# Kernel tuning notes

Hardware: AMD Instinct MI355X
Metric: run time of the kernel (lower is better)

## Reference

```python
import jax, jax.numpy as jnp
import numpy as np

KH = KW = 3
PAD = 1


def _conv2d(x, w, b):
    y = jax.lax.conv_general_dilated(
        x, w, window_strides=(1, 1), padding=((PAD, PAD), (PAD, PAD)),
        dimension_numbers=("NCHW", "OIHW", "NCHW"))
    return y + b[None, :, None, None]


def _bilinear_sample_one(img, ys, xs):
    # img: [C,H,W]; ys,xs: [K,h,w] absolute sampling coords; zeros outside.
    C, H, W = img.shape
    flat = img.reshape(C, H * W)
    y0 = jnp.floor(ys)
    x0 = jnp.floor(xs)
    wy = ys - y0
    wx = xs - x0

    def gather(yi, xi):
        valid = (yi >= 0) & (yi <= H - 1) & (xi >= 0) & (xi <= W - 1)
        yc = jnp.clip(yi, 0, H - 1).astype(jnp.int32)
        xc = jnp.clip(xi, 0, W - 1).astype(jnp.int32)
        idx = (yc * W + xc).reshape(-1)
        v = jnp.take(flat, idx, axis=1).reshape((C,) + yi.shape)
        return v * valid.astype(img.dtype)

    v00 = gather(y0, x0)
    v01 = gather(y0, x0 + 1)
    v10 = gather(y0 + 1, x0)
    v11 = gather(y0 + 1, x0 + 1)
    return (v00 * (1 - wy) * (1 - wx) + v01 * (1 - wy) * wx
            + v10 * wy * (1 - wx) + v11 * wy * wx)  # [C,K,h,w]


def deform_conv2d(x, offset, weight, bias):
    # x: [B,C,H,W]; offset: [B,2K,h,w] with (dy,dx) per tap; stride 1, pad 1.
    B, C, H, W = x.shape
    h, w = offset.shape[2], offset.shape[3]
    K = KH * KW
    off = offset.reshape(B, K, 2, h, w)
    ky = (jnp.arange(K) // KW - PAD).astype(x.dtype)  # tap row displacement
    kx = (jnp.arange(K) % KW - PAD).astype(x.dtype)
    ii = jnp.arange(h, dtype=x.dtype)[None, :, None]
    jj = jnp.arange(w, dtype=x.dtype)[None, None, :]
    ys = ii - PAD + ky[:, None, None] + off[:, :, 0]  # [B,K,h,w]
    xs = jj - PAD + kx[:, None, None] + off[:, :, 1]
    sampled = jax.vmap(_bilinear_sample_one)(x, ys, xs)  # [B,C,K,h,w]
    Co = weight.shape[0]
    out = jnp.einsum('ock,bckhw->bohw', weight.reshape(Co, C, K), sampled)
    return out + bias[None, :, None, None]


def setup_inputs() -> dict:
    key = jax.random.key(0)
    ks = jax.random.split(key, 5)
    B, C, H, W = 4, 64, 128, 128
    x = jax.random.normal(ks[0], (B, C, H, W), dtype=jnp.float32)
    w_off = jax.random.normal(ks[1], (4, C, KH, KW), dtype=jnp.float32) * 0.05
    b_off = jnp.zeros((4,), dtype=jnp.float32)
    weight = jax.random.normal(ks[2], (C, C, KH, KW), dtype=jnp.float32) * 0.05
    bias = jnp.zeros((C,), dtype=jnp.float32)
    # base_offset: canonical 3x3 tap displacements, layout (dy,dx) per tap.
    ky = np.repeat(np.arange(KH) - PAD, KW).astype(np.float32)
    kx = np.tile(np.arange(KW) - PAD, KH).astype(np.float32)
    base = np.stack([ky, kx], axis=1).reshape(-1)  # [18]
    base_offset = jnp.asarray(np.broadcast_to(base[None, :, None, None], (1, 18, H, W)).copy())
    idx = np.arange(18)
    mask1 = jnp.asarray(idx % 2 == 0)  # y coords -> scale1
    mask2 = jnp.asarray(idx % 2 == 1)  # x coords -> scale2
    return {"x": x, "w_off": w_off, "b_off": b_off, "weight": weight,
            "bias": bias, "base_offset": base_offset, "mask1": mask1, "mask2": mask2}


def reference(x, w_off, b_off, weight, bias, base_offset, mask1, mask2):
    off = _conv2d(x, w_off, b_off)  # [B,4,h,w]
    scale1 = jax.nn.relu(off[:, 2:3]) + 1.0  # [B,1,h,w]
    scale2 = jax.nn.relu(off[:, 3:4]) + 1.0
    shift = jnp.tile(off[:, :2], (1, KH * KW, 1, 1))  # [B,18,h,w]
    # scaled_offset[:, mask1] = base*scale1 ; scaled_offset[:, mask2] = base*scale2
    scale_full = jnp.where(mask1[None, :, None, None], scale1, scale2)  # [B,18,h,w]
    offset = base_offset * scale_full - base_offset + shift
    return deform_conv2d(x, offset, weight, bias)
```

## Files before the change

kernel.cpp:

```cpp
#include <hip/hip_runtime.h>

#define Hd 128
#define Wd 128
#define Cd 64
#define COd 64
#define Bd 4
#define HWd (Hd*Wd)

typedef __attribute__((ext_vector_type(8))) _Float16 half8;
typedef __attribute__((ext_vector_type(2))) _Float16 h2;
typedef __attribute__((ext_vector_type(4))) float    f32x4;

__device__ __align__(16) _Float16 g_wh[COd*576];
__device__ __align__(16) _Float16 g_woffh[16*576];
__device__ float4 g_offs[Bd*HWd];
__device__ __align__(16) unsigned short g_xt[(size_t)Bd*HWd*Cd];

static __device__ __forceinline__ unsigned cvtpkh(float lo, float hi) {
    unsigned r;
    asm("v_cvt_pkrtz_f16_f32 %0, %1, %2" : "=v"(r) : "v"(lo), "v"(hi));
    return r;
}
static __device__ __forceinline__ h2 ash2(unsigned u) {
    union { unsigned u; h2 h; } x; x.u = u; return x.h;
}
static __device__ __forceinline__ unsigned ash2u(h2 h) {
    union { h2 h; unsigned u; } x; x.h = h; return x.u;
}

__global__ __launch_bounds__(256) void k_prep(const float* __restrict__ x,
                                              const float* __restrict__ weight,
                                              const float* __restrict__ w_off) {
    int bid = blockIdx.x;
    if (bid < 512) {
        int b = bid >> 7, y = bid & 127;
        int px = threadIdx.x & 127;
        int h  = threadIdx.x >> 7;
        const float* xb = x + (size_t)b*Cd*HWd + y*Wd + px;
        unsigned short* ob = g_xt + ((size_t)(b*HWd) + y*Wd + px)*Cd + h*32;
        #pragma unroll
        for (int oct = 0; oct < 4; ++oct) {
            unsigned pk[4];
            #pragma unroll
            for (int e = 0; e < 4; ++e) {
                float v0 = xb[(size_t)(h*32 + oct*8 + 2*e    )*HWd];
                float v1 = xb[(size_t)(h*32 + oct*8 + 2*e + 1)*HWd];
                pk[e] = cvtpkh(v0, v1);
            }
            *(uint4*)(ob + oct*8) = make_uint4(pk[0], pk[1], pk[2], pk[3]);
        }
    } else if (bid < 656) {
        int g = (bid - 512)*256 + threadIdx.x;
        if (g < COd*576) {
            int co = g / 576, k = g % 576;
            int t = k >> 6, c = k & 63;
            g_wh[g] = (_Float16)weight[(co*Cd + c)*9 + t];
        }
    } else {
        int g = (bid - 656)*256 + threadIdx.x;
        if (g < 16*576) {
            int row = g / 576, k = g % 576;
            int t = k >> 6, c = k & 63;
            g_woffh[g] = (row < 4) ? (_Float16)w_off[(row*Cd + c)*9 + t] : (_Float16)0.f;
        }
    }
}

__global__ __launch_bounds__(256) void k_offs(const float* __restrict__ b_off) {
    int orig = blockIdx.x;
    int xcd = orig & 7, slot = orig >> 3;
    int g = xcd*2 + (slot >> 6);
    int s = slot & 63;
    int b  = g >> 2;
    int i  = (g & 3)*32 + (s >> 1);
    int j0 = (s & 1) << 6;

    int w  = threadIdx.x >> 6;
    int l  = threadIdx.x & 63;
    int pc = l & 15, q = l >> 4;
    int j  = j0 + w*16 + pc;

    const unsigned short* xb = g_xt + (size_t)b*HWd*Cd;
    const _Float16* arow = g_woffh + pc*576 + q*8;

    f32x4 acc = {0.f, 0.f, 0.f, 0.f};
    #pragma unroll
    for (int t = 0; t < 9; ++t) {
        int yy = i + t/3 - 1, xx = j + t%3 - 1;
        bool ok = (yy >= 0) & (yy <= 127) & (xx >= 0) & (xx <= 127);
        const unsigned short* p = xb + (size_t)(yy*Wd + xx)*Cd + q*8;
        uint4 u0 = ok ? *(const uint4*)p        : make_uint4(0,0,0,0);
        uint4 u1 = ok ? *(const uint4*)(p + 32) : make_uint4(0,0,0,0);
        half8 b0 = *(half8*)&u0;
        half8 b1 = *(half8*)&u1;
        half8 a0 = *(const half8*)(arow + (2*t    )*32);
        half8 a1 = *(const half8*)(arow + (2*t + 1)*32);
        acc = __builtin_amdgcn_mfma_f32_16x16x32_f16(a0, b0, acc, 0, 0, 0);
        acc = __builtin_amdgcn_mfma_f32_16x16x32_f16(a1, b1, acc, 0, 0, 0);
    }
    if (q == 0) {
        float o0 = acc[0] + b_off[0];
        float o1 = acc[1] + b_off[1];
        float o2 = fmaxf(acc[2] + b_off[2], 0.f) + 1.f;
        float o3 = fmaxf(acc[3] + b_off[3], 0.f) + 1.f;
        g_offs[(b*Hd + i)*Wd + j] = make_float4(o0, o1, o2, o3);
    }
}

#define GATHER(T, U00, U01, U10, U11, H00, H01, H10, H11)                         \
    {                                                                             \
        float ys = (float)(i - 1) + (float)((T)/3 - 1)*s1v + off0;                \
        float xs = (float)(jA - 1) + (float)((T)%3 - 1)*s2v + off1;               \
        float y0f = floorf(ys), x0f = floorf(xs);                                 \
        float wy = ys - y0f, wx = xs - x0f;                                       \
        float vy0 = (y0f >=  0.f && y0f <= 127.f) ? 1.f : 0.f;                    \
        float vy1 = (y0f >= -1.f && y0f <= 126.f) ? 1.f : 0.f;                    \
        float vx0 = (x0f >=  0.f && x0f <= 127.f) ? 1.f : 0.f;                    \
        float vx1 = (x0f >= -1.f && x0f <= 126.f) ? 1.f : 0.f;                    \
        float w00 = (1.f-wy)*(1.f-wx)*vy0*vx0, w01 = (1.f-wy)*wx*vy0*vx1;         \
        float w10 = wy*(1.f-wx)*vy1*vx0,       w11 = wy*wx*vy1*vx1;               \
        H00 = ash2(cvtpkh(w00, w00)); H01 = ash2(cvtpkh(w01, w01));               \
        H10 = ash2(cvtpkh(w10, w10)); H11 = ash2(cvtpkh(w11, w11));               \
        int iy0 = min(max((int)y0f,     0), 127), iy1 = min(max((int)y0f+1,0),127);\
        int ix0 = min(max((int)x0f,     0), 127), ix1 = min(max((int)x0f+1,0),127);\
        U00 = *(const uint4*)(xb + (size_t)(iy0*Wd + ix0)*Cd + oct*8);            \
        U01 = *(const uint4*)(xb + (size_t)(iy0*Wd + ix1)*Cd + oct*8);            \
        U10 = *(const uint4*)(xb + (size_t)(iy1*Wd + ix0)*Cd + oct*8);            \
        U11 = *(const uint4*)(xb + (size_t)(iy1*Wd + ix1)*Cd + oct*8);            \
    }

#define PACK_STORE(BUF, U00, U01, U10, U11, H00, H01, H10, H11)                   \
    {                                                                             \
        unsigned a00[4] = {U00.x,U00.y,U00.z,U00.w};                              \
        unsigned a01[4] = {U01.x,U01.y,U01.z,U01.w};                              \
        unsigned a10[4] = {U10.x,U10.y,U10.z,U10.w};                              \
        unsigned a11[4] = {U11.x,U11.y,U11.z,U11.w};                              \
        unsigned pk[4];                                                           \
        _Pragma("unroll")                                                         \
        for (int e = 0; e < 4; ++e) {                                             \
            h2 r = ash2(a00[e])*H00 + ash2(a01[e])*H01                            \
                 + ash2(a10[e])*H10 + ash2(a11[e])*H11;                           \
            pk[e] = ash2u(r);                                                     \
        }                                                                         \
        lds_b[(((BUF)*2 + par)*2 + nt)*64 + slotA] = make_uint4(pk[0],pk[1],pk[2],pk[3]); \
    }

__global__ __launch_bounds__(256) void k_deform(const float* __restrict__ bias,
                                                float* __restrict__ out) {
    __shared__ uint4 lds_b[2*2*2*64];
    int orig = blockIdx.x;
    int xcd = orig & 7, slotB = orig >> 3;
    int g = xcd*2 + (slotB >> 7);
    int s = slotB & 127;
    int b = g >> 2;
    int i = (g & 3)*32 + (s >> 2);
    int j0 = (s & 3) << 5;

    int w = threadIdx.x >> 6, l = threadIdx.x & 63;
    int oct = l & 7, px8 = l >> 3;
    int pxl = w*8 + px8;
    int jA  = j0 + pxl;
    int nt = pxl >> 4, pcA = pxl & 15, qA = oct & 3, par = oct >> 2;
    int slotA = (pcA ^ (qA << 1)) + (qA << 4);
    int pcB = l & 15, qB = l >> 4;
    int physl = (pcB ^ (qB << 1)) + (qB << 4);
    const _Float16* wrow = g_wh + (size_t)(w*16 + pcB)*576 + qB*8;

    const unsigned short* xb = g_xt + (size_t)b*HWd*Cd;
    float4 o4 = g_offs[(b*Hd + i)*Wd + jA];
    float off0 = o4.x, off1 = o4.y, s1v = o4.z, s2v = o4.w;

    f32x4 acc0 = {0.f,0.f,0.f,0.f};
    f32x4 acc1 = {0.f,0.f,0.f,0.f};

    uint4 gc00, gc01, gc10, gc11, gn00, gn01, gn10, gn11;
    h2 hc00, hc01, hc10, hc11, hn00, hn01, hn10, hn11;
    half8 ac0, ac1, an0, an1;

    GATHER(0, gc00, gc01, gc10, gc11, hc00, hc01, hc10, hc11);
    ac0 = *(const half8*)(wrow + 0*32);
    ac1 = *(const half8*)(wrow + 1*32);

    #pragma unroll
    for (int t = 0; t < 9; ++t) {
        if (t < 8) {
            GATHER(t+1, gn00, gn01, gn10, gn11, hn00, hn01, hn10, hn11);
            an0 = *(const half8*)(wrow + (2*t + 2)*32);
            an1 = *(const half8*)(wrow + (2*t + 3)*32);
        }
        PACK_STORE(t & 1, gc00, gc01, gc10, gc11, hc00, hc01, hc10, hc11);
        __syncthreads();
        {
            half8 b00 = *(const half8*)&lds_b[(((t&1)*2 + 0)*2 + 0)*64 + physl];
            half8 b01 = *(const half8*)&lds_b[(((t&1)*2 + 0)*2 + 1)*64 + physl];
            half8 b10 = *(const half8*)&lds_b[(((t&1)*2 + 1)*2 + 0)*64 + physl];
            half8 b11 = *(const half8*)&lds_b[(((t&1)*2 + 1)*2 + 1)*64 + physl];
            acc0 = __builtin_amdgcn_mfma_f32_16x16x32_f16(ac0, b00, acc0, 0, 0, 0);
            acc1 = __builtin_amdgcn_mfma_f32_16x16x32_f16(ac0, b01, acc1, 0, 0, 0);
            acc0 = __builtin_amdgcn_mfma_f32_16x16x32_f16(ac1, b10, acc0, 0, 0, 0);
            acc1 = __builtin_amdgcn_mfma_f32_16x16x32_f16(ac1, b11, acc1, 0, 0, 0);
        }
        if (t < 8) {
            gc00 = gn00; gc01 = gn01; gc10 = gn10; gc11 = gn11;
            hc00 = hn00; hc01 = hn01; hc10 = hn10; hc11 = hn11;
            ac0 = an0; ac1 = an1;
        }
    }

    #pragma unroll
    for (int rr = 0; rr < 4; ++rr) {
        int co = w*16 + qB*4 + rr;
        float bco = bias[co];
        size_t base = ((size_t)(b*COd + co)*Hd + i)*Wd + j0;
        out[base + pcB]      = acc0[rr] + bco;
        out[base + 16 + pcB] = acc1[rr] + bco;
    }
}

extern "C" void kernel_launch(void* const* d_in, const int* in_sizes, int n_in,
                              void* d_out, int out_size, void* d_ws, size_t ws_size,
                              hipStream_t stream) {
    const float* x      = (const float*)d_in[0];
    const float* w_off  = (const float*)d_in[1];
    const float* b_off  = (const float*)d_in[2];
    const float* weight = (const float*)d_in[3];
    const float* bias   = (const float*)d_in[4];
    float* out = (float*)d_out;

    hipLaunchKernelGGL(k_prep,   dim3(692),  dim3(256), 0, stream, x, weight, w_off);
    hipLaunchKernelGGL(k_offs,   dim3(1024), dim3(256), 0, stream, b_off);
    hipLaunchKernelGGL(k_deform, dim3(2048), dim3(256), 0, stream, bias, out);
}
```

Before: 59.68 us.

## Fuse offset conv into deform kernel with per-wave tiles and no block barrier

Merges the offset-prediction conv and the deformable conv into one kernel. Each wave computes offsets for its own 16 pixels with MFMA and passes them to the sampling lanes by shuffle, so the global offsets buffer and one launch go away. Each wave now owns 16 pixels across all 64 output channels and uses a private swizzled LDS region, which removes the block-wide __syncthreads. In exchange, weight A-fragments are reloaded from global memory for each tap and channel group, and register pressure rises under launch bounds of 4 blocks.

```diff
diff --git a/kernel.cpp b/kernel.cpp
--- a/kernel.cpp
+++ b/kernel.cpp
@@ -13,7 +13,6 @@
 
 __device__ __align__(16) _Float16 g_wh[COd*576];
 __device__ __align__(16) _Float16 g_woffh[16*576];
-__device__ float4 g_offs[Bd*HWd];
 __device__ __align__(16) unsigned short g_xt[(size_t)Bd*HWd*Cd];
 
 static __device__ __forceinline__ unsigned cvtpkh(float lo, float hi) {
@@ -66,7 +65,10 @@
     }
 }
 
-__global__ __launch_bounds__(256) void k_offs(const float* __restrict__ b_off) {
+__global__ __launch_bounds__(256, 4) void k_main(const float* __restrict__ b_off,
+                                                 const float* __restrict__ bias,
+                                                 float* __restrict__ out) {
+    __shared__ uint4 lds[4*2*128];
     int orig = blockIdx.x;
     int xcd = orig & 7, slot = orig >> 3;
     int g = xcd*2 + (slot >> 6);
@@ -75,145 +77,139 @@
     int i  = (g & 3)*32 + (s >> 1);
     int j0 = (s & 1) << 6;
 
-    int w  = threadIdx.x >> 6;
-    int l  = threadIdx.x & 63;
+    int w = threadIdx.x >> 6, l = threadIdx.x & 63;
+    int p0 = j0 + w*16;
+    const unsigned short* xb = g_xt + (size_t)b*HWd*Cd;
+    uint4* lw = lds + w*256;
+
     int pc = l & 15, q = l >> 4;
-    int j  = j0 + w*16 + pc;
-
-    const unsigned short* xb = g_xt + (size_t)b*HWd*Cd;
-    const _Float16* arow = g_woffh + pc*576 + q*8;
-
-    f32x4 acc = {0.f, 0.f, 0.f, 0.f};
+
+    f32x4 oacc = {0.f, 0.f, 0.f, 0.f};
+    {
+        int jh = p0 + pc;
+        const _Float16* arow = g_woffh + pc*576 + q*8;
+        #pragma unroll
+        for (int t = 0; t < 9; ++t) {
+            int yy = i + t/3 - 1, xx = jh + t%3 - 1;
+            bool ok = (yy >= 0) & (yy <= 127) & (xx >= 0) & (xx <= 127);
+            const unsigned short* p = xb + (size_t)(yy*Wd + xx)*Cd + q*8;
+            uint4 u0 = ok ? *(const uint4*)p        : make_uint4(0,0,0,0);
+            uint4 u1 = ok ? *(const uint4*)(p + 32) : make_uint4(0,0,0,0);
+            half8 a0 = *(const half8*)(arow + (2*t    )*32);
+            half8 a1 = *(const half8*)(arow + (2*t + 1)*32);
+            oacc = __builtin_amdgcn_mfma_f32_16x16x32_f16(a0, *(half8*)&u0, oacc, 0, 0, 0);
+            oacc = __builtin_amdgcn_mfma_f32_16x16x32_f16(a1, *(half8*)&u1, oacc, 0, 0, 0);
+        }
+    }
+    int oct = l & 7, px8 = l >> 3;
+    int s0i = px8, s1i = 8 + px8;
+    float off0_0 = __shfl(oacc[0], s0i, 64) + b_off[0];
+    float off1_0 = __shfl(oacc[1], s0i, 64) + b_off[1];
+    float sc1_0  = fmaxf(__shfl(oacc[2], s0i, 64) + b_off[2], 0.f) + 1.f;
+    float sc2_0  = fmaxf(__shfl(oacc[3], s0i, 64) + b_off[3], 0.f) + 1.f;
+    float off0_1 = __shfl(oacc[0], s1i, 64) + b_off[0];
+    float off1_1 = __shfl(oacc[1], s1i, 64) + b_off[1];
+    float sc1_1  = fmaxf(__shfl(oacc[2], s1i, 64) + b_off[2], 0.f) + 1.f;
+    float sc2_1  = fmaxf(__shfl(oacc[3], s1i, 64) + b_off[3], 0.f) + 1.f;
+
+    int jr0 = p0 + px8, jr1 = p0 + 8 + px8;
+    int swz = px8 & 7;
+
+    f32x4 accm[4];
+    #pragma unroll
+    for (int cg = 0; cg < 4; ++cg) accm[cg] = (f32x4){0.f, 0.f, 0.f, 0.f};
+
     #pragma unroll
     for (int t = 0; t < 9; ++t) {
-        int yy = i + t/3 - 1, xx = j + t%3 - 1;
-        bool ok = (yy >= 0) & (yy <= 127) & (xx >= 0) & (xx <= 127);
-        const unsigned short* p = xb + (size_t)(yy*Wd + xx)*Cd + q*8;
-        uint4 u0 = ok ? *(const uint4*)p        : make_uint4(0,0,0,0);
-        uint4 u1 = ok ? *(const uint4*)(p + 32) : make_uint4(0,0,0,0);
-        half8 b0 = *(half8*)&u0;
-        half8 b1 = *(half8*)&u1;
-        half8 a0 = *(const half8*)(arow + (2*t    )*32);
-        half8 a1 = *(const half8*)(arow + (2*t + 1)*32);
-        acc = __builtin_amdgcn_mfma_f32_16x16x32_f16(a0, b0, acc, 0, 0, 0);
-        acc = __builtin_amdgcn_mfma_f32_16x16x32_f16(a1, b1, acc, 0, 0, 0);
-    }
-    if (q == 0) {
-        float o0 = acc[0] + b_off[0];
-        float o1 = acc[1] + b_off[1];
-        float o2 = fmaxf(acc[2] + b_off[2], 0.f) + 1.f;
-        float o3 = fmaxf(acc[3] + b_off[3], 0.f) + 1.f;
-        g_offs[(b*Hd + i)*Wd + j] = make_float4(o0, o1, o2, o3);
-    }
-}
-
-#define GATHER(T, U00, U01, U10, U11, H00, H01, H10, H11)                         \
-    {                                                                             \
-        float ys = (float)(i - 1) + (float)((T)/3 - 1)*s1v + off0;                \
-        float xs = (float)(jA - 1) + (float)((T)%3 - 1)*s2v + off1;               \
-        float y0f = floorf(ys), x0f = floorf(xs);                                 \
-        float wy = ys - y0f, wx = xs - x0f;                                       \
-        float vy0 = (y0f >=  0.f && y0f <= 127.f) ? 1.f : 0.f;                    \
-        float vy1 = (y0f >= -1.f && y0f <= 126.f) ? 1.f : 0.f;                    \
-        float vx0 = (x0f >=  0.f && x0f <= 127.f) ? 1.f : 0.f;                    \
-        float vx1 = (x0f >= -1.f && x0f <= 126.f) ? 1.f : 0.f;                    \
-        float w00 = (1.f-wy)*(1.f-wx)*vy0*vx0, w01 = (1.f-wy)*wx*vy0*vx1;         \
-        float w10 = wy*(1.f-wx)*vy1*vx0,       w11 = wy*wx*vy1*vx1;               \
-        H00 = ash2(cvtpkh(w00, w00)); H01 = ash2(cvtpkh(w01, w01));               \
-        H10 = ash2(cvtpkh(w10, w10)); H11 = ash2(cvtpkh(w11, w11));               \
-        int iy0 = min(max((int)y0f,     0), 127), iy1 = min(max((int)y0f+1,0),127);\
-        int ix0 = min(max((int)x0f,     0), 127), ix1 = min(max((int)x0f+1,0),127);\
-        U00 = *(const uint4*)(xb + (size_t)(iy0*Wd + ix0)*Cd + oct*8);            \
-        U01 = *(const uint4*)(xb + (size_t)(iy0*Wd + ix1)*Cd + oct*8);            \
-        U10 = *(const uint4*)(xb + (size_t)(iy1*Wd + ix0)*Cd + oct*8);            \
-        U11 = *(const uint4*)(xb + (size_t)(iy1*Wd + ix1)*Cd + oct*8);            \
-    }
-
-#define PACK_STORE(BUF, U00, U01, U10, U11, H00, H01, H10, H11)                   \
-    {                                                                             \
-        unsigned a00[4] = {U00.x,U00.y,U00.z,U00.w};                              \
-        unsigned a01[4] = {U01.x,U01.y,U01.z,U01.w};                              \
-        unsigned a10[4] = {U10.x,U10.y,U10.z,U10.w};                              \
-        unsigned a11[4] = {U11.x,U11.y,U11.z,U11.w};                              \
-        unsigned pk[4];                                                           \
-        _Pragma("unroll")                                                         \
-        for (int e = 0; e < 4; ++e) {                                             \
-            h2 r = ash2(a00[e])*H00 + ash2(a01[e])*H01                            \
-                 + ash2(a10[e])*H10 + ash2(a11[e])*H11;                           \
-            pk[e] = ash2u(r);                                                     \
-        }                                                                         \
-        lds_b[(((BUF)*2 + par)*2 + nt)*64 + slotA] = make_uint4(pk[0],pk[1],pk[2],pk[3]); \
-    }
-
-__global__ __launch_bounds__(256) void k_deform(const float* __restrict__ bias,
-                                                float* __restrict__ out) {
-    __shared__ uint4 lds_b[2*2*2*64];
-    int orig = blockIdx.x;
-    int xcd = orig & 7, slotB = orig >> 3;
-    int g = xcd*2 + (slotB >> 7);
-    int s = slotB & 127;
-    int b = g >> 2;
-    int i = (g & 3)*32 + (s >> 2);
-    int j0 = (s & 3) << 5;
-
-    int w = threadIdx.x >> 6, l = threadIdx.x & 63;
-    int oct = l & 7, px8 = l >> 3;
-    int pxl = w*8 + px8;
-    int jA  = j0 + pxl;
-    int nt = pxl >> 4, pcA = pxl & 15, qA = oct & 3, par = oct >> 2;
-    int slotA = (pcA ^ (qA << 1)) + (qA << 4);
-    int pcB = l & 15, qB = l >> 4;
-    int physl = (pcB ^ (qB << 1)) + (qB << 4);
-    const _Float16* wrow = g_wh + (size_t)(w*16 + pcB)*576 + qB*8;
-
-    const unsigned short* xb = g_xt + (size_t)b*HWd*Cd;
-    float4 o4 = g_offs[(b*Hd + i)*Wd + jA];
-    float off0 = o4.x, off1 = o4.y, s1v = o4.z, s2v = o4.w;
-
-    f32x4 acc0 = {0.f,0.f,0.f,0.f};
-    f32x4 acc1 = {0.f,0.f,0.f,0.f};
-
-    uint4 gc00, gc01, gc10, gc11, gn00, gn01, gn10, gn11;
-    h2 hc00, hc01, hc10, hc11, hn00, hn01, hn10, hn11;
-    half8 ac0, ac1, an0, an1;
-
-    GATHER(0, gc00, gc01, gc10, gc11, hc00, hc01, hc10, hc11);
-    ac0 = *(const half8*)(wrow + 0*32);
-    ac1 = *(const half8*)(wrow + 1*32);
+        const float ky = (float)(t/3 - 1), kx = (float)(t%3 - 1);
+        uint4 u00, u01, u10, u11, v00, v01, v10, v11;
+        h2 H00, H01, H10, H11, G00, G01, G10, G11;
+        {
+            float ys = (float)(i - 1) + ky*sc1_0 + off0_0;
+            float xs = (float)(jr0 - 1) + kx*sc2_0 + off1_0;
+            float y0f = floorf(ys), x0f = floorf(xs);
+            float wy = ys - y0f, wx = xs - x0f;
+            float vy0 = (y0f >=  0.f && y0f <= 127.f) ? 1.f : 0.f;
+            float vy1 = (y0f >= -1.f && y0f <= 126.f) ? 1.f : 0.f;
+            float vx0 = (x0f >=  0.f && x0f <= 127.f) ? 1.f : 0.f;
+            float vx1 = (x0f >= -1.f && x0f <= 126.f) ? 1.f : 0.f;
+            float w00 = (1.f-wy)*(1.f-wx)*vy0*vx0, w01 = (1.f-wy)*wx*vy0*vx1;
+            float w10 = wy*(1.f-wx)*vy1*vx0,       w11 = wy*wx*vy1*vx1;
+            H00 = ash2(cvtpkh(w00, w00)); H01 = ash2(cvtpkh(w01, w01));
+            H10 = ash2(cvtpkh(w10, w10)); H11 = ash2(cvtpkh(w11, w11));
+            int iy0 = min(max((int)y0f, 0), 127), iy1 = min(max((int)y0f + 1, 0), 127);
+            int ix0 = min(max((int)x0f, 0), 127), ix1 = min(max((int)x0f + 1, 0), 127);
+            u00 = *(const uint4*)(xb + (size_t)(iy0*Wd + ix0)*Cd + oct*8);
+            u01 = *(const uint4*)(xb + (size_t)(iy0*Wd + ix1)*Cd + oct*8);
+            u10 = *(const uint4*)(xb + (size_t)(iy1*Wd + ix0)*Cd + oct*8);
+            u11 = *(const uint4*)(xb + (size_t)(iy1*Wd + ix1)*Cd + oct*8);
+        }
+        {
+            float ys = (float)(i - 1) + ky*sc1_1 + off0_1;
+            float xs = (float)(jr1 - 1) + kx*sc2_1 + off1_1;
+            float y0f = floorf(ys), x0f = floorf(xs);
+            float wy = ys - y0f, wx = xs - x0f;
+            float vy0 = (y0f >=  0.f && y0f <= 127.f) ? 1.f : 0.f;
+            float vy1 = (y0f >= -1.f && y0f <= 126.f) ? 1.f : 0.f;
+            float vx0 = (x0f >=  0.f && x0f <= 127.f) ? 1.f : 0.f;
+            float vx1 = (x0f >= -1.f && x0f <= 126.f) ? 1.f : 0.f;
+            float w00 = (1.f-wy)*(1.f-wx)*vy0*vx0, w01 = (1.f-wy)*wx*vy0*vx1;
+            float w10 = wy*(1.f-wx)*vy1*vx0,       w11 = wy*wx*vy1*vx1;
+            G00 = ash2(cvtpkh(w00, w00)); G01 = ash2(cvtpkh(w01, w01));
+            G10 = ash2(cvtpkh(w10, w10)); G11 = ash2(cvtpkh(w11, w11));
+            int iy0 = min(max((int)y0f, 0), 127), iy1 = min(max((int)y0f + 1, 0), 127);
+            int ix0 = min(max((int)x0f, 0), 127), ix1 = min(max((int)x0f + 1, 0), 127);
+            v00 = *(const uint4*)(xb + (size_t)(iy0*Wd + ix0)*Cd + oct*8);
+            v01 = *(const uint4*)(xb + (size_t)(iy0*Wd + ix1)*Cd + oct*8);
+            v10 = *(const uint4*)(xb + (size_t)(iy1*Wd + ix0)*Cd + oct*8);
+            v11 = *(const uint4*)(xb + (size_t)(iy1*Wd + ix1)*Cd + oct*8);
+        }
+        {
+            unsigned a00[4] = {u00.x,u00.y,u00.z,u00.w}, a01[4] = {u01.x,u01.y,u01.z,u01.w};
+            unsigned a10[4] = {u10.x,u10.y,u10.z,u10.w}, a11[4] = {u11.x,u11.y,u11.z,u11.w};
+            unsigned pk[4];
+            #pragma unroll
+            for (int e = 0; e < 4; ++e) {
+                h2 r = ash2(a00[e])*H00 + ash2(a01[e])*H01
+                     + ash2(a10[e])*H10 + ash2(a11[e])*H11;
+                pk[e] = ash2u(r);
+            }
+            lw[(t&1)*128 + px8*8 + (oct ^ swz)] = make_uint4(pk[0], pk[1], pk[2], pk[3]);
+        }
+        {
+            unsigned a00[4] = {v00.x,v00.y,v00.z,v00.w}, a01[4] = {v01.x,v01.y,v01.z,v01.w};
+            unsigned a10[4] = {v10.x,v10.y,v10.z,v10.w}, a11[4] = {v11.x,v11.y,v11.z,v11.w};
+            unsigned pk[4];
+            #pragma unroll
+            for (int e = 0; e < 4; ++e) {
+                h2 r = ash2(a00[e])*G00 + ash2(a01[e])*G01
+                     + ash2(a10[e])*G10 + ash2(a11[e])*G11;
+                pk[e] = ash2u(r);
+            }
+            lw[(t&1)*128 + (8 + px8)*8 + (oct ^ swz)] = make_uint4(pk[0], pk[1], pk[2], pk[3]);
+        }
+        #pragma unroll
+        for (int ks2 = 0; ks2 < 2; ++ks2) {
+            int hg = ks2*4 + q;
+            uint4 bu = lw[(t&1)*128 + pc*8 + (hg ^ (pc & 7))];
+            half8 bf = *(half8*)&bu;
+            #pragma unroll
+            for (int cg = 0; cg < 4; ++cg) {
+                half8 av = *(const half8*)(g_wh + (size_t)(cg*16 + pc)*576 + (2*t + ks2)*32 + q*8);
+                accm[cg] = __builtin_amdgcn_mfma_f32_16x16x32_f16(av, bf, accm[cg], 0, 0, 0);
+            }
+        }
+    }
 
     #pragma unroll
-    for (int t = 0; t < 9; ++t) {
-        if (t < 8) {
-            GATHER(t+1, gn00, gn01, gn10, gn11, hn00, hn01, hn10, hn11);
-            an0 = *(const half8*)(wrow + (2*t + 2)*32);
-            an1 = *(const half8*)(wrow + (2*t + 3)*32);
-        }
-        PACK_STORE(t & 1, gc00, gc01, gc10, gc11, hc00, hc01, hc10, hc11);
-        __syncthreads();
-        {
-            half8 b00 = *(const half8*)&lds_b[(((t&1)*2 + 0)*2 + 0)*64 + physl];
-            half8 b01 = *(const half8*)&lds_b[(((t&1)*2 + 0)*2 + 1)*64 + physl];
-            half8 b10 = *(const half8*)&lds_b[(((t&1)*2 + 1)*2 + 0)*64 + physl];
-            half8 b11 = *(const half8*)&lds_b[(((t&1)*2 + 1)*2 + 1)*64 + physl];
-            acc0 = __builtin_amdgcn_mfma_f32_16x16x32_f16(ac0, b00, acc0, 0, 0, 0);
-            acc1 = __builtin_amdgcn_mfma_f32_16x16x32_f16(ac0, b01, acc1, 0, 0, 0);
-            acc0 = __builtin_amdgcn_mfma_f32_16x16x32_f16(ac1, b10, acc0, 0, 0, 0);
-            acc1 = __builtin_amdgcn_mfma_f32_16x16x32_f16(ac1, b11, acc1, 0, 0, 0);
-        }
-        if (t < 8) {
-            gc00 = gn00; gc01 = gn01; gc10 = gn10; gc11 = gn11;
-            hc00 = hn00; hc01 = hn01; hc10 = hn10; hc11 = hn11;
-            ac0 = an0; ac1 = an1;
-        }
-    }
-
-    #pragma unroll
-    for (int rr = 0; rr < 4; ++rr) {
-        int co = w*16 + qB*4 + rr;
-        float bco = bias[co];
-        size_t base = ((size_t)(b*COd + co)*Hd + i)*Wd + j0;
-        out[base + pcB]      = acc0[rr] + bco;
-        out[base + 16 + pcB] = acc1[rr] + bco;
+    for (int cg = 0; cg < 4; ++cg) {
+        float4 bv = *(const float4*)(bias + cg*16 + q*4);
+        float bb[4] = {bv.x, bv.y, bv.z, bv.w};
+        #pragma unroll
+        for (int rr = 0; rr < 4; ++rr) {
+            int co = cg*16 + q*4 + rr;
+            out[((size_t)(b*COd + co)*Hd + i)*Wd + p0 + pc] = accm[cg][rr] + bb[rr];
+        }
     }
 }
 
@@ -227,7 +223,6 @@
     const float* bias   = (const float*)d_in[4];
     float* out = (float*)d_out;
 
-    hipLaunchKernelGGL(k_prep,   dim3(692),  dim3(256), 0, stream, x, weight, w_off);
-    hipLaunchKernelGGL(k_offs,   dim3(1024), dim3(256), 0, stream, b_off);
-    hipLaunchKernelGGL(k_deform, dim3(2048), dim3(256), 0, stream, bias, out);
-}
+    hipLaunchKernelGGL(k_prep, dim3(692),  dim3(256), 0, stream, x, weight, w_off);
+    hipLaunchKernelGGL(k_main, dim3(1024), dim3(256), 0, stream, b_off, bias, out);
+}
```

New measurement: 79.86 us. +33.8%, slower.

## Fuse three kernels into one cooperative persistent kernel with grid syncs

Applied to the files above, without the earlier changes.

Merges the prep, offset-conv and deformable-conv kernels into a single cooperative launch. The grid is sized from occupancy and capped at 2048, and each stage is separated by grid.sync(). The goal is to remove the launch gaps between kernels. Weight fragments are no longer prefetched one tap ahead but loaded inside the loop body. The cost is grid-sync overhead, and if fewer blocks are resident than the stage block counts, the persistent loops serialise that work. The occupancy query also runs on the host at every launch.

```diff
diff --git a/kernel.cpp b/kernel.cpp
--- a/kernel.cpp
+++ b/kernel.cpp
@@ -1,4 +1,5 @@
 #include <hip/hip_runtime.h>
+#include <hip/hip_cooperative_groups.h>
 
 #define Hd 128
 #define Wd 128
@@ -7,6 +8,8 @@
 #define Bd 4
 #define HWd (Hd*Wd)
 
+namespace cg = cooperative_groups;
+
 typedef __attribute__((ext_vector_type(8))) _Float16 half8;
 typedef __attribute__((ext_vector_type(2))) _Float16 h2;
 typedef __attribute__((ext_vector_type(4))) float    f32x4;
@@ -26,85 +29,6 @@
 }
 static __device__ __forceinline__ unsigned ash2u(h2 h) {
     union { h2 h; unsigned u; } x; x.h = h; return x.u;
-}
-
-__global__ __launch_bounds__(256) void k_prep(const float* __restrict__ x,
-                                              const float* __restrict__ weight,
-                                              const float* __restrict__ w_off) {
-    int bid = blockIdx.x;
-    if (bid < 512) {
-        int b = bid >> 7, y = bid & 127;
-        int px = threadIdx.x & 127;
-        int h  = threadIdx.x >> 7;
-        const float* xb = x + (size_t)b*Cd*HWd + y*Wd + px;
-        unsigned short* ob = g_xt + ((size_t)(b*HWd) + y*Wd + px)*Cd + h*32;
-        #pragma unroll
-        for (int oct = 0; oct < 4; ++oct) {
-            unsigned pk[4];
-            #pragma unroll
-            for (int e = 0; e < 4; ++e) {
-                float v0 = xb[(size_t)(h*32 + oct*8 + 2*e    )*HWd];
-                float v1 = xb[(size_t)(h*32 + oct*8 + 2*e + 1)*HWd];
-                pk[e] = cvtpkh(v0, v1);
-            }
-            *(uint4*)(ob + oct*8) = make_uint4(pk[0], pk[1], pk[2], pk[3]);
-        }
-    } else if (bid < 656) {
-        int g = (bid - 512)*256 + threadIdx.x;
-        if (g < COd*576) {
-            int co = g / 576, k = g % 576;
-            int t = k >> 6, c = k & 63;
-            g_wh[g] = (_Float16)weight[(co*Cd + c)*9 + t];
-        }
-    } else {
-        int g = (bid - 656)*256 + threadIdx.x;
-        if (g < 16*576) {
-            int row = g / 576, k = g % 576;
-            int t = k >> 6, c = k & 63;
-            g_woffh[g] = (row < 4) ? (_Float16)w_off[(row*Cd + c)*9 + t] : (_Float16)0.f;
-        }
-    }
-}
-
-__global__ __launch_bounds__(256) void k_offs(const float* __restrict__ b_off) {
-    int orig = blockIdx.x;
-    int xcd = orig & 7, slot = orig >> 3;
-    int g = xcd*2 + (slot >> 6);
-    int s = slot & 63;
-    int b  = g >> 2;
-    int i  = (g & 3)*32 + (s >> 1);
-    int j0 = (s & 1) << 6;
-
-    int w  = threadIdx.x >> 6;
-    int l  = threadIdx.x & 63;
-    int pc = l & 15, q = l >> 4;
-    int j  = j0 + w*16 + pc;
-
-    const unsigned short* xb = g_xt + (size_t)b*HWd*Cd;
-    const _Float16* arow = g_woffh + pc*576 + q*8;
-
-    f32x4 acc = {0.f, 0.f, 0.f, 0.f};
-    #pragma unroll
-    for (int t = 0; t < 9; ++t) {
-        int yy = i + t/3 - 1, xx = j + t%3 - 1;
-        bool ok = (yy >= 0) & (yy <= 127) & (xx >= 0) & (xx <= 127);
-        const unsigned short* p = xb + (size_t)(yy*Wd + xx)*Cd + q*8;
-        uint4 u0 = ok ? *(const uint4*)p        : make_uint4(0,0,0,0);
-        uint4 u1 = ok ? *(const uint4*)(p + 32) : make_uint4(0,0,0,0);
-        half8 b0 = *(half8*)&u0;
-        half8 b1 = *(half8*)&u1;
-        half8 a0 = *(const half8*)(arow + (2*t    )*32);
-        half8 a1 = *(const half8*)(arow + (2*t + 1)*32);
-        acc = __builtin_amdgcn_mfma_f32_16x16x32_f16(a0, b0, acc, 0, 0, 0);
-        acc = __builtin_amdgcn_mfma_f32_16x16x32_f16(a1, b1, acc, 0, 0, 0);
-    }
-    if (q == 0) {
-        float o0 = acc[0] + b_off[0];
-        float o1 = acc[1] + b_off[1];
-        float o2 = fmaxf(acc[2] + b_off[2], 0.f) + 1.f;
-        float o3 = fmaxf(acc[3] + b_off[3], 0.f) + 1.f;
-        g_offs[(b*Hd + i)*Wd + j] = make_float4(o0, o1, o2, o3);
-    }
 }
 
 #define GATHER(T, U00, U01, U10, U11, H00, H01, H10, H11)                         \
@@ -145,75 +69,150 @@
         lds_b[(((BUF)*2 + par)*2 + nt)*64 + slotA] = make_uint4(pk[0],pk[1],pk[2],pk[3]); \
     }
 
-__global__ __launch_bounds__(256) void k_deform(const float* __restrict__ bias,
-                                                float* __restrict__ out) {
+__global__ __launch_bounds__(256)
+void k_coop(const float* __restrict__ x, const float* __restrict__ w_off,
+            const float* __restrict__ b_off, const float* __restrict__ bias,
+            const float* __restrict__ weight, float* __restrict__ out) {
     __shared__ uint4 lds_b[2*2*2*64];
-    int orig = blockIdx.x;
-    int xcd = orig & 7, slotB = orig >> 3;
-    int g = xcd*2 + (slotB >> 7);
-    int s = slotB & 127;
-    int b = g >> 2;
-    int i = (g & 3)*32 + (s >> 2);
-    int j0 = (s & 3) << 5;
-
-    int w = threadIdx.x >> 6, l = threadIdx.x & 63;
-    int oct = l & 7, px8 = l >> 3;
-    int pxl = w*8 + px8;
-    int jA  = j0 + pxl;
-    int nt = pxl >> 4, pcA = pxl & 15, qA = oct & 3, par = oct >> 2;
-    int slotA = (pcA ^ (qA << 1)) + (qA << 4);
-    int pcB = l & 15, qB = l >> 4;
-    int physl = (pcB ^ (qB << 1)) + (qB << 4);
-    const _Float16* wrow = g_wh + (size_t)(w*16 + pcB)*576 + qB*8;
-
-    const unsigned short* xb = g_xt + (size_t)b*HWd*Cd;
-    float4 o4 = g_offs[(b*Hd + i)*Wd + jA];
-    float off0 = o4.x, off1 = o4.y, s1v = o4.z, s2v = o4.w;
-
-    f32x4 acc0 = {0.f,0.f,0.f,0.f};
-    f32x4 acc1 = {0.f,0.f,0.f,0.f};
-
-    uint4 gc00, gc01, gc10, gc11, gn00, gn01, gn10, gn11;
-    h2 hc00, hc01, hc10, hc11, hn00, hn01, hn10, hn11;
-    half8 ac0, ac1, an0, an1;
-
-    GATHER(0, gc00, gc01, gc10, gc11, hc00, hc01, hc10, hc11);
-    ac0 = *(const half8*)(wrow + 0*32);
-    ac1 = *(const half8*)(wrow + 1*32);
-
-    #pragma unroll
-    for (int t = 0; t < 9; ++t) {
-        if (t < 8) {
-            GATHER(t+1, gn00, gn01, gn10, gn11, hn00, hn01, hn10, hn11);
-            an0 = *(const half8*)(wrow + (2*t + 2)*32);
-            an1 = *(const half8*)(wrow + (2*t + 3)*32);
-        }
-        PACK_STORE(t & 1, gc00, gc01, gc10, gc11, hc00, hc01, hc10, hc11);
+    cg::grid_group gridg = cg::this_grid();
+    const int nb  = gridDim.x;
+    const int tid = threadIdx.x;
+
+    for (int bid = blockIdx.x; bid < 692; bid += nb) {
+        if (bid < 512) {
+            int b = bid >> 7, y = bid & 127;
+            int px = tid & 127;
+            int h  = tid >> 7;
+            const float* xb = x + (size_t)b*Cd*HWd + y*Wd + px;
+            unsigned short* ob = g_xt + ((size_t)(b*HWd) + y*Wd + px)*Cd + h*32;
+            #pragma unroll
+            for (int oct = 0; oct < 4; ++oct) {
+                unsigned pk[4];
+                #pragma unroll
+                for (int e = 0; e < 4; ++e) {
+                    float v0 = xb[(size_t)(h*32 + oct*8 + 2*e    )*HWd];
+                    float v1 = xb[(size_t)(h*32 + oct*8 + 2*e + 1)*HWd];
+                    pk[e] = cvtpkh(v0, v1);
+                }
+                *(uint4*)(ob + oct*8) = make_uint4(pk[0], pk[1], pk[2], pk[3]);
+            }
+        } else if (bid < 656) {
+            int gg = (bid - 512)*256 + tid;
+            if (gg < COd*576) {
+                int co = gg / 576, k = gg % 576;
+                int t = k >> 6, c = k & 63;
+                g_wh[gg] = (_Float16)weight[(co*Cd + c)*9 + t];
+            }
+        } else {
+            int gg = (bid - 656)*256 + tid;
+            if (gg < 16*576) {
+                int row = gg / 576, k = gg % 576;
+                int t = k >> 6, c = k & 63;
+                g_woffh[gg] = (row < 4) ? (_Float16)w_off[(row*Cd + c)*9 + t] : (_Float16)0.f;
+            }
+        }
+    }
+    gridg.sync();
+
+    for (int orig = blockIdx.x; orig < 1024; orig += nb) {
+        int xcd = orig & 7, slot = orig >> 3;
+        int gq = xcd*2 + (slot >> 6);
+        int sq = slot & 63;
+        int b  = gq >> 2;
+        int i  = (gq & 3)*32 + (sq >> 1);
+        int j0 = (sq & 1) << 6;
+        int w  = tid >> 6, l = tid & 63;
+        int pc = l & 15, q = l >> 4;
+        int j  = j0 + w*16 + pc;
+        const unsigned short* xb = g_xt + (size_t)b*HWd*Cd;
+        const _Float16* arow = g_woffh + pc*576 + q*8;
+        f32x4 acc = {0.f, 0.f, 0.f, 0.f};
+        #pragma unroll
+        for (int t = 0; t < 9; ++t) {
+            int yy = i + t/3 - 1, xx = j + t%3 - 1;
+            bool ok = (yy >= 0) & (yy <= 127) & (xx >= 0) & (xx <= 127);
+            const unsigned short* p = xb + (size_t)(yy*Wd + xx)*Cd + q*8;
+            uint4 u0 = ok ? *(const uint4*)p        : make_uint4(0,0,0,0);
+            uint4 u1 = ok ? *(const uint4*)(p + 32) : make_uint4(0,0,0,0);
+            half8 a0 = *(const half8*)(arow + (2*t    )*32);
+            half8 a1 = *(const half8*)(arow + (2*t + 1)*32);
+            acc = __builtin_amdgcn_mfma_f32_16x16x32_f16(a0, *(half8*)&u0, acc, 0, 0, 0);
+            acc = __builtin_amdgcn_mfma_f32_16x16x32_f16(a1, *(half8*)&u1, acc, 0, 0, 0);
+        }
+        if (q == 0) {
+            float o0 = acc[0] + b_off[0];
+            float o1 = acc[1] + b_off[1];
+            float o2 = fmaxf(acc[2] + b_off[2], 0.f) + 1.f;
+            float o3 = fmaxf(acc[3] + b_off[3], 0.f) + 1.f;
+            g_offs[(b*Hd + i)*Wd + j] = make_float4(o0, o1, o2, o3);
+        }
+    }
+    gridg.sync();
+
+    for (int orig = blockIdx.x; orig < 2048; orig += nb) {
+        int xcd = orig & 7, slotB = orig >> 3;
+        int gq = xcd*2 + (slotB >> 7);
+        int sq = slotB & 127;
+        int b  = gq >> 2;
+        int i  = (gq & 3)*32 + (sq >> 2);
+        int j0 = (sq & 3) << 5;
+
+        int w = tid >> 6, l = tid & 63;
+        int oct = l & 7, px8 = l >> 3;
+        int pxl = w*8 + px8;
+        int jA  = j0 + pxl;
+        int nt = pxl >> 4, pcA = pxl & 15, qA = oct & 3, par = oct >> 2;
+        int slotA = (pcA ^ (qA << 1)) + (qA << 4);
+        int pcB = l & 15, qB = l >> 4;
+        int physl = (pcB ^ (qB << 1)) + (qB << 4);
+        const _Float16* wrow = g_wh + (size_t)(w*16 + pcB)*576 + qB*8;
+
+        const unsigned short* xb = g_xt + (size_t)b*HWd*Cd;
+        float4 o4 = g_offs[(b*Hd + i)*Wd + jA];
+        float off0 = o4.x, off1 = o4.y, s1v = o4.z, s2v = o4.w;
+
+        f32x4 acc0 = {0.f,0.f,0.f,0.f};
+        f32x4 acc1 = {0.f,0.f,0.f,0.f};
+
+        uint4 gc00, gc01, gc10, gc11, gn00, gn01, gn10, gn11;
+        h2 hc00, hc01, hc10, hc11, hn00, hn01, hn10, hn11;
+
+        GATHER(0, gc00, gc01, gc10, gc11, hc00, hc01, hc10, hc11);
+
+        #pragma unroll
+        for (int t = 0; t < 9; ++t) {
+            if (t < 8) {
+                GATHER(t+1, gn00, gn01, gn10, gn11, hn00, hn01, hn10, hn11);
+            }
+            PACK_STORE(t & 1, gc00, gc01, gc10, gc11, hc00, hc01, hc10, hc11);
+            __syncthreads();
+            {
+                half8 a0 = *(const half8*)(wrow + (2*t    )*32);
+                half8 a1 = *(const half8*)(wrow + (2*t + 1)*32);
+                half8 b00 = *(const half8*)&lds_b[(((t&1)*2 + 0)*2 + 0)*64 + physl];
+                half8 b01 = *(const half8*)&lds_b[(((t&1)*2 + 0)*2 + 1)*64 + physl];
+                half8 b10 = *(const half8*)&lds_b[(((t&1)*2 + 1)*2 + 0)*64 + physl];
+                half8 b11 = *(const half8*)&lds_b[(((t&1)*2 + 1)*2 + 1)*64 + physl];
+                acc0 = __builtin_amdgcn_mfma_f32_16x16x32_f16(a0, b00, acc0, 0, 0, 0);
+                acc1 = __builtin_amdgcn_mfma_f32_16x16x32_f16(a0, b01, acc1, 0, 0, 0);
+                acc0 = __builtin_amdgcn_mfma_f32_16x16x32_f16(a1, b10, acc0, 0, 0, 0);
+                acc1 = __builtin_amdgcn_mfma_f32_16x16x32_f16(a1, b11, acc1, 0, 0, 0);
+            }
+            if (t < 8) {
+                gc00 = gn00; gc01 = gn01; gc10 = gn10; gc11 = gn11;
+                hc00 = hn00; hc01 = hn01; hc10 = hn10; hc11 = hn11;
+            }
+        }
+
+        #pragma unroll
+        for (int rr = 0; rr < 4; ++rr) {
+            int co = w*16 + qB*4 + rr;
+            float bco = bias[co];
+            size_t base = ((size_t)(b*COd + co)*Hd + i)*Wd + j0;
+            out[base + pcB]      = acc0[rr] + bco;
+            out[base + 16 + pcB] = acc1[rr] + bco;
+        }
         __syncthreads();
-        {
-            half8 b00 = *(const half8*)&lds_b[(((t&1)*2 + 0)*2 + 0)*64 + physl];
-            half8 b01 = *(const half8*)&lds_b[(((t&1)*2 + 0)*2 + 1)*64 + physl];
-            half8 b10 = *(const half8*)&lds_b[(((t&1)*2 + 1)*2 + 0)*64 + physl];
-            half8 b11 = *(const half8*)&lds_b[(((t&1)*2 + 1)*2 + 1)*64 + physl];
-            acc0 = __builtin_amdgcn_mfma_f32_16x16x32_f16(ac0, b00, acc0, 0, 0, 0);
-            acc1 = __builtin_amdgcn_mfma_f32_16x16x32_f16(ac0, b01, acc1, 0, 0, 0);
-            acc0 = __builtin_amdgcn_mfma_f32_16x16x32_f16(ac1, b10, acc0, 0, 0, 0);
-            acc1 = __builtin_amdgcn_mfma_f32_16x16x32_f16(ac1, b11, acc1, 0, 0, 0);
-        }
-        if (t < 8) {
-            gc00 = gn00; gc01 = gn01; gc10 = gn10; gc11 = gn11;
-            hc00 = hn00; hc01 = hn01; hc10 = hn10; hc11 = hn11;
-            ac0 = an0; ac1 = an1;
-        }
-    }
-
-    #pragma unroll
-    for (int rr = 0; rr < 4; ++rr) {
-        int co = w*16 + qB*4 + rr;
-        float bco = bias[co];
-        size_t base = ((size_t)(b*COd + co)*Hd + i)*Wd + j0;
-        out[base + pcB]      = acc0[rr] + bco;
-        out[base + 16 + pcB] = acc1[rr] + bco;
     }
 }
 
@@ -227,7 +226,14 @@
     const float* bias   = (const float*)d_in[4];
     float* out = (float*)d_out;
 
-    hipLaunchKernelGGL(k_prep,   dim3(692),  dim3(256), 0, stream, x, weight, w_off);
-    hipLaunchKernelGGL(k_offs,   dim3(1024), dim3(256), 0, stream, b_off);
-    hipLaunchKernelGGL(k_deform, dim3(2048), dim3(256), 0, stream, bias, out);
-}
+    int maxb = 0;
+    hipOccupancyMaxActiveBlocksPerMultiprocessor(&maxb, (const void*)k_coop, 256, 0);
+    if (maxb < 1) maxb = 1;
+    long long grid = (long long)maxb * 256;
+    if (grid > 2048) grid = 2048;
+
+    void* params[6] = { (void*)&x, (void*)&w_off, (void*)&b_off,
+                        (void*)&bias, (void*)&weight, (void*)&out };
+    hipLaunchCooperativeKernel((const void*)k_coop, dim3((unsigned)grid), dim3(256),
+                               params, 0, stream);
+}
```

Result: slower. 185.3 us (+210.6%).

## Fuse offset convolution into deform kernel via shared memory

Applied to the files above, without the earlier changes.

Removes the separate offset-conv kernel and its global float4 offset buffer. Each deform block's first two waves now compute the offset conv for its 32 pixels with MFMA and hand the results to all waves through LDS after a barrier. This saves a launch and the global round trip, but the other two waves sit idle during that phase, adding a serial prologue. Separately, the weight-fragment loads are no longer prefetched one tap ahead and are instead loaded right before the MFMAs, which lowers register pressure but exposes load latency.

```diff
diff --git a/kernel.cpp b/kernel.cpp
--- a/kernel.cpp
+++ b/kernel.cpp
@@ -13,7 +13,6 @@
 
 __device__ __align__(16) _Float16 g_wh[COd*576];
 __device__ __align__(16) _Float16 g_woffh[16*576];
-__device__ float4 g_offs[Bd*HWd];
 __device__ __align__(16) unsigned short g_xt[(size_t)Bd*HWd*Cd];
 
 static __device__ __forceinline__ unsigned cvtpkh(float lo, float hi) {
@@ -66,47 +65,6 @@
     }
 }
 
-__global__ __launch_bounds__(256) void k_offs(const float* __restrict__ b_off) {
-    int orig = blockIdx.x;
-    int xcd = orig & 7, slot = orig >> 3;
-    int g = xcd*2 + (slot >> 6);
-    int s = slot & 63;
-    int b  = g >> 2;
-    int i  = (g & 3)*32 + (s >> 1);
-    int j0 = (s & 1) << 6;
-
-    int w  = threadIdx.x >> 6;
-    int l  = threadIdx.x & 63;
-    int pc = l & 15, q = l >> 4;
-    int j  = j0 + w*16 + pc;
-
-    const unsigned short* xb = g_xt + (size_t)b*HWd*Cd;
-    const _Float16* arow = g_woffh + pc*576 + q*8;
-
-    f32x4 acc = {0.f, 0.f, 0.f, 0.f};
-    #pragma unroll
-    for (int t = 0; t < 9; ++t) {
-        int yy = i + t/3 - 1, xx = j + t%3 - 1;
-        bool ok = (yy >= 0) & (yy <= 127) & (xx >= 0) & (xx <= 127);
-        const unsigned short* p = xb + (size_t)(yy*Wd + xx)*Cd + q*8;
-        uint4 u0 = ok ? *(const uint4*)p        : make_uint4(0,0,0,0);
-        uint4 u1 = ok ? *(const uint4*)(p + 32) : make_uint4(0,0,0,0);
-        half8 b0 = *(half8*)&u0;
-        half8 b1 = *(half8*)&u1;
-        half8 a0 = *(const half8*)(arow + (2*t    )*32);
-        half8 a1 = *(const half8*)(arow + (2*t + 1)*32);
-        acc = __builtin_amdgcn_mfma_f32_16x16x32_f16(a0, b0, acc, 0, 0, 0);
-        acc = __builtin_amdgcn_mfma_f32_16x16x32_f16(a1, b1, acc, 0, 0, 0);
-    }
-    if (q == 0) {
-        float o0 = acc[0] + b_off[0];
-        float o1 = acc[1] + b_off[1];
-        float o2 = fmaxf(acc[2] + b_off[2], 0.f) + 1.f;
-        float o3 = fmaxf(acc[3] + b_off[3], 0.f) + 1.f;
-        g_offs[(b*Hd + i)*Wd + j] = make_float4(o0, o1, o2, o3);
-    }
-}
-
 #define GATHER(T, U00, U01, U10, U11, H00, H01, H10, H11)                         \
     {                                                                             \
         float ys = (float)(i - 1) + (float)((T)/3 - 1)*s1v + off0;                \
@@ -145,9 +103,11 @@
         lds_b[(((BUF)*2 + par)*2 + nt)*64 + slotA] = make_uint4(pk[0],pk[1],pk[2],pk[3]); \
     }
 
-__global__ __launch_bounds__(256) void k_deform(const float* __restrict__ bias,
+__global__ __launch_bounds__(256) void k_deform(const float* __restrict__ b_off,
+                                                const float* __restrict__ bias,
                                                 float* __restrict__ out) {
-    __shared__ uint4 lds_b[2*2*2*64];
+    __shared__ uint4  lds_b[2*2*2*64];
+    __shared__ float4 lds_off[32];
     int orig = blockIdx.x;
     int xcd = orig & 7, slotB = orig >> 3;
     int g = xcd*2 + (slotB >> 7);
@@ -157,6 +117,35 @@
     int j0 = (s & 3) << 5;
 
     int w = threadIdx.x >> 6, l = threadIdx.x & 63;
+    const unsigned short* xb = g_xt + (size_t)b*HWd*Cd;
+
+    if (w < 2) {
+        int pc = l & 15, q = l >> 4;
+        int j  = j0 + w*16 + pc;
+        const _Float16* arow = g_woffh + pc*576 + q*8;
+        f32x4 acc = {0.f, 0.f, 0.f, 0.f};
+        #pragma unroll
+        for (int t = 0; t < 9; ++t) {
+            int yy = i + t/3 - 1, xx = j + t%3 - 1;
+            bool ok = (yy >= 0) & (yy <= 127) & (xx >= 0) & (xx <= 127);
+            const unsigned short* p = xb + (size_t)(yy*Wd + xx)*Cd + q*8;
+            uint4 u0 = ok ? *(const uint4*)p        : make_uint4(0,0,0,0);
+            uint4 u1 = ok ? *(const uint4*)(p + 32) : make_uint4(0,0,0,0);
+            half8 a0 = *(const half8*)(arow + (2*t    )*32);
+            half8 a1 = *(const half8*)(arow + (2*t + 1)*32);
+            acc = __builtin_amdgcn_mfma_f32_16x16x32_f16(a0, *(half8*)&u0, acc, 0, 0, 0);
+            acc = __builtin_amdgcn_mfma_f32_16x16x32_f16(a1, *(half8*)&u1, acc, 0, 0, 0);
+        }
+        if (q == 0) {
+            float o0 = acc[0] + b_off[0];
+            float o1 = acc[1] + b_off[1];
+            float o2 = fmaxf(acc[2] + b_off[2], 0.f) + 1.f;
+            float o3 = fmaxf(acc[3] + b_off[3], 0.f) + 1.f;
+            lds_off[w*16 + pc] = make_float4(o0, o1, o2, o3);
+        }
+    }
+    __syncthreads();
+
     int oct = l & 7, px8 = l >> 3;
     int pxl = w*8 + px8;
     int jA  = j0 + pxl;
@@ -166,8 +155,7 @@
     int physl = (pcB ^ (qB << 1)) + (qB << 4);
     const _Float16* wrow = g_wh + (size_t)(w*16 + pcB)*576 + qB*8;
 
-    const unsigned short* xb = g_xt + (size_t)b*HWd*Cd;
-    float4 o4 = g_offs[(b*Hd + i)*Wd + jA];
+    float4 o4 = lds_off[pxl];
     float off0 = o4.x, off1 = o4.y, s1v = o4.z, s2v = o4.w;
 
     f32x4 acc0 = {0.f,0.f,0.f,0.f};
@@ -175,35 +163,31 @@
 
     uint4 gc00, gc01, gc10, gc11, gn00, gn01, gn10, gn11;
     h2 hc00, hc01, hc10, hc11, hn00, hn01, hn10, hn11;
-    half8 ac0, ac1, an0, an1;
 
     GATHER(0, gc00, gc01, gc10, gc11, hc00, hc01, hc10, hc11);
-    ac0 = *(const half8*)(wrow + 0*32);
-    ac1 = *(const half8*)(wrow + 1*32);
 
     #pragma unroll
     for (int t = 0; t < 9; ++t) {
         if (t < 8) {
             GATHER(t+1, gn00, gn01, gn10, gn11, hn00, hn01, hn10, hn11);
-            an0 = *(const half8*)(wrow + (2*t + 2)*32);
-            an1 = *(const half8*)(wrow + (2*t + 3)*32);
         }
         PACK_STORE(t & 1, gc00, gc01, gc10, gc11, hc00, hc01, hc10, hc11);
         __syncthreads();
         {
+            half8 a0 = *(const half8*)(wrow + (2*t    )*32);
+            half8 a1 = *(const half8*)(wrow + (2*t + 1)*32);
             half8 b00 = *(const half8*)&lds_b[(((t&1)*2 + 0)*2 + 0)*64 + physl];
             half8 b01 = *(const half8*)&lds_b[(((t&1)*2 + 0)*2 + 1)*64 + physl];
             half8 b10 = *(const half8*)&lds_b[(((t&1)*2 + 1)*2 + 0)*64 + physl];
             half8 b11 = *(const half8*)&lds_b[(((t&1)*2 + 1)*2 + 1)*64 + physl];
-            acc0 = __builtin_amdgcn_mfma_f32_16x16x32_f16(ac0, b00, acc0, 0, 0, 0);
-            acc1 = __builtin_amdgcn_mfma_f32_16x16x32_f16(ac0, b01, acc1, 0, 0, 0);
-            acc0 = __builtin_amdgcn_mfma_f32_16x16x32_f16(ac1, b10, acc0, 0, 0, 0);
-            acc1 = __builtin_amdgcn_mfma_f32_16x16x32_f16(ac1, b11, acc1, 0, 0, 0);
+            acc0 = __builtin_amdgcn_mfma_f32_16x16x32_f16(a0, b00, acc0, 0, 0, 0);
+            acc1 = __builtin_amdgcn_mfma_f32_16x16x32_f16(a0, b01, acc1, 0, 0, 0);
+            acc0 = __builtin_amdgcn_mfma_f32_16x16x32_f16(a1, b10, acc0, 0, 0, 0);
+            acc1 = __builtin_amdgcn_mfma_f32_16x16x32_f16(a1, b11, acc1, 0, 0, 0);
         }
         if (t < 8) {
             gc00 = gn00; gc01 = gn01; gc10 = gn10; gc11 = gn11;
             hc00 = hn00; hc01 = hn01; hc10 = hn10; hc11 = hn11;
-            ac0 = an0; ac1 = an1;
         }
     }
 
@@ -228,6 +212,5 @@
     float* out = (float*)d_out;
 
     hipLaunchKernelGGL(k_prep,   dim3(692),  dim3(256), 0, stream, x, weight, w_off);
-    hipLaunchKernelGGL(k_offs,   dim3(1024), dim3(256), 0, stream, b_off);
-    hipLaunchKernelGGL(k_deform, dim3(2048), dim3(256), 0, stream, bias, out);
-}
+    hipLaunchKernelGGL(k_deform, dim3(2048), dim3(256), 0, stream, b_off, bias, out);
+}
```

New measurement: 62.18 us. 1.04x slower.
